# Kernel tuning notes

Hardware: AMD Instinct MI355X
Metric: run time of the kernel (lower is better)

## Reference

```python
import jax, jax.numpy as jnp
import numpy as np

T_LEN, E_LEN, BATCH, DIM = 32, 256, 16, 512  # topic_len, exp_len, batch, input=hidden size
HID = 512


def setup_inputs() -> dict:
    key = jax.random.key(0)
    k1, k2, k3, k4, k5, k6 = jax.random.split(key, 6)
    topic = jax.random.normal(k1, (T_LEN, BATCH, DIM), dtype=jnp.float32)
    exp_output = jax.random.normal(k2, (E_LEN, BATCH, DIM), dtype=jnp.float32)
    seq_mask = jax.random.bernoulli(k3, 0.1, (E_LEN, BATCH))  # True = masked exp position
    # nn.Linear(hidden+input, hidden): weight [HID, HID+DIM], bias [HID]
    lim1 = 1.0 / np.sqrt(HID + DIM)
    W_attn = jax.random.uniform(k4, (HID, HID + DIM), minval=-lim1, maxval=lim1, dtype=jnp.float32)
    b_attn = jax.random.uniform(k5, (HID,), minval=-lim1, maxval=lim1, dtype=jnp.float32)
    # nn.Linear(hidden, 1): weight [1, HID], bias [1]
    lim2 = 1.0 / np.sqrt(HID)
    kv, kb = jax.random.split(k6)
    v_score = jax.random.uniform(kv, (1, HID), minval=-lim2, maxval=lim2, dtype=jnp.float32)
    b_score = jax.random.uniform(kb, (1,), minval=-lim2, maxval=lim2, dtype=jnp.float32)
    return {"topic": topic, "exp_output": exp_output, "seq_mask": seq_mask,
            "W_attn": W_attn, "b_attn": b_attn, "v_score": v_score, "b_score": b_score}


def reference(topic, exp_output, seq_mask, W_attn, b_attn, v_score, b_score):
    # topic: [T, B, D]; exp_output: [E, B, D]; seq_mask: [E, B] bool
    D = topic.shape[2]
    # Split the concat-Linear: cat(topic, exp) @ W.T == topic @ W[:, :D].T + exp @ W[:, D:].T
    proj_t = jnp.einsum('tbd,hd->bth', topic, W_attn[:, :D])        # [B, T, H]
    proj_e = jnp.einsum('ebd,hd->beh', exp_output, W_attn[:, D:])   # [B, E, H]
    feat = jnp.tanh(proj_t[:, :, None, :] + proj_e[:, None, :, :] + b_attn)  # [B, T, E, H]
    energies = jnp.einsum('bteh,h->bte', feat, v_score[0]) + b_score[0]      # [B, T, E]
    # mask exp positions (broadcast over topic dim), as masked_fill(-1e12)
    energies = jnp.where(seq_mask.T[:, None, :], jnp.float32(-1e12), energies)
    attn_s1 = jax.nn.softmax(jnp.swapaxes(energies, 1, 2), axis=2)  # [B, E, T], softmax over topics
    attn_s2 = jax.nn.softmax(energies, axis=2)                      # [B, T, E], softmax over exp
    new_exp = jnp.einsum('bet,btd->bed', attn_s1, jnp.swapaxes(topic, 0, 1))       # [B, E, D]
    new_topic = jnp.einsum('bte,bed->btd', attn_s2, jnp.swapaxes(exp_output, 0, 1))  # [B, T, D]
    return new_topic, new_exp
```

## Files before the change

### kernel.cpp

```cpp
#include <hip/hip_runtime.h>
#include <hip/hip_bf16.h>
#include <cstddef>
#include <cstdint>

#define T_LEN 32
#define E_LEN 256
#define BATCH 16
#define DIM 512
#define HID 512
#define WROW 1024

#define TWO_LOG2E 2.8853900817779268f

typedef __attribute__((ext_vector_type(8))) short bf16x8;
typedef __attribute__((ext_vector_type(4))) float f32x4;

__device__ inline bf16x8 cvt8(float4 a, float4 b) {
    union { bf16x8 v; __hip_bfloat16 h[8]; } u;
    u.h[0] = __float2bfloat16(a.x); u.h[1] = __float2bfloat16(a.y);
    u.h[2] = __float2bfloat16(a.z); u.h[3] = __float2bfloat16(a.w);
    u.h[4] = __float2bfloat16(b.x); u.h[5] = __float2bfloat16(b.y);
    u.h[6] = __float2bfloat16(b.z); u.h[7] = __float2bfloat16(b.w);
    return u.v;
}

#define GPAD 8
#define GLDR (64 + GPAD)

__global__ __launch_bounds__(256) void gemm_fused(
    const float* __restrict__ topic, const float* __restrict__ expo,
    const float* __restrict__ W, const float* __restrict__ battn,
    float* __restrict__ EPT, float* __restrict__ EPE) {
    __shared__ __hip_bfloat16 As[64 * GLDR];
    __shared__ __hip_bfloat16 Bs[64 * GLDR];
    const int tid = threadIdx.x;
    const int by = blockIdx.y;
    const float* A; const float* Wp; const float* bias; float* C; int m0;
    if (by < 8) { A = topic; Wp = W;       bias = battn;   C = EPT; m0 = by * 64; }
    else        { A = expo;  Wp = W + DIM; bias = nullptr; C = EPE; m0 = (by - 8) * 64; }
    const int n0 = blockIdx.x * 64;
    const int w = tid >> 6;
    const int lane = tid & 63;
    const int l15 = lane & 15;
    const int g = lane >> 4;
    const int srow = tid >> 2;
    const int sc = tid & 3;

    f32x4 acc[4];
    const f32x4 z = {0.f, 0.f, 0.f, 0.f};
#pragma unroll
    for (int nt = 0; nt < 4; ++nt) acc[nt] = z;

    const float* ga = A + (size_t)(m0 + srow) * 512 + sc * 8;
    const float* gb = Wp + (size_t)(n0 + srow) * WROW + sc * 8;

    float4 a0 = *(const float4*)(ga);
    float4 a1 = *(const float4*)(ga + 4);
    float4 a2 = *(const float4*)(ga + 32);
    float4 a3 = *(const float4*)(ga + 36);
    float4 b0 = *(const float4*)(gb);
    float4 b1 = *(const float4*)(gb + 4);
    float4 b2 = *(const float4*)(gb + 32);
    float4 b3 = *(const float4*)(gb + 36);

    for (int kk = 0; kk < 8; ++kk) {
        bf16x8 av0 = cvt8(a0, a1), av1 = cvt8(a2, a3);
        bf16x8 bv0 = cvt8(b0, b1), bv1 = cvt8(b2, b3);
        if (kk < 7) {
            ga += 64; gb += 64;
            a0 = *(const float4*)(ga);
            a1 = *(const float4*)(ga + 4);
            a2 = *(const float4*)(ga + 32);
            a3 = *(const float4*)(ga + 36);
            b0 = *(const float4*)(gb);
            b1 = *(const float4*)(gb + 4);
            b2 = *(const float4*)(gb + 32);
            b3 = *(const float4*)(gb + 36);
        }
        __syncthreads();
        *(bf16x8*)&As[srow * GLDR + sc * 8] = av0;
        *(bf16x8*)&As[srow * GLDR + sc * 8 + 32] = av1;
        *(bf16x8*)&Bs[srow * GLDR + sc * 8] = bv0;
        *(bf16x8*)&Bs[srow * GLDR + sc * 8 + 32] = bv1;
        __syncthreads();
#pragma unroll
        for (int s = 0; s < 2; ++s) {
            bf16x8 af = *(const bf16x8*)&As[(w * 16 + l15) * GLDR + (s * 4 + g) * 8];
#pragma unroll
            for (int nt = 0; nt < 4; ++nt) {
                bf16x8 bf = *(const bf16x8*)&Bs[(nt * 16 + l15) * GLDR + (s * 4 + g) * 8];
                acc[nt] = __builtin_amdgcn_mfma_f32_16x16x32_bf16(af, bf, acc[nt], 0, 0, 0);
            }
        }
    }
#pragma unroll
    for (int nt = 0; nt < 4; ++nt) {
        int n = n0 + nt * 16 + l15;
        float bv = bias ? bias[n] : 0.f;
#pragma unroll
        for (int r = 0; r < 4; ++r) {
            int m = m0 + w * 16 + g * 4 + r;
            C[(size_t)m * 512 + n] = __builtin_amdgcn_exp2f((acc[nt][r] + bv) * TWO_LOG2E);
        }
    }
}

__global__ __launch_bounds__(256) void energies_k(const float* __restrict__ EPT,
                                                  const float* __restrict__ EPE,
                                                  const float* __restrict__ v,
                                                  const float* __restrict__ bscore,
                                                  const int* __restrict__ mask,
                                                  float* __restrict__ EN) {
    const int b = blockIdx.x;
    const int tg = blockIdx.y;
    const int ech = blockIdx.z;
    const int lane = threadIdx.x & 63;
    const int w = threadIdx.x >> 6;
    const int h0 = lane * 8;

    float sv[8], spt[4][8];
    float sumv;
    {
        float4 v0 = *(const float4*)(v + h0);
        float4 v1 = *(const float4*)(v + h0 + 4);
        float vr[8] = {v0.x, v0.y, v0.z, v0.w, v1.x, v1.y, v1.z, v1.w};
        float s = 0.f;
#pragma unroll
        for (int j = 0; j < 8; ++j) { sv[j] = -2.f * vr[j]; s += vr[j]; }
#pragma unroll
        for (int off = 32; off; off >>= 1) s += __shfl_xor(s, off);
        sumv = s;
#pragma unroll
        for (int i = 0; i < 4; ++i) {
            const float* p = EPT + ((size_t)((tg * 4 + i) * BATCH + b)) * HID + h0;
            float4 p0 = *(const float4*)(p);
            float4 p1 = *(const float4*)(p + 4);
            spt[i][0] = p0.x; spt[i][1] = p0.y; spt[i][2] = p0.z; spt[i][3] = p0.w;
            spt[i][4] = p1.x; spt[i][5] = p1.y; spt[i][6] = p1.z; spt[i][7] = p1.w;
        }
    }
    const int e0 = ech * 16 + w * 4;
    const float bs = bscore[0];
#pragma unroll
    for (int ei = 0; ei < 4; ++ei) {
        const int e = e0 + ei;
        const float* pe = EPE + ((size_t)(e * BATCH + b)) * HID + h0;
        float4 p0 = *(const float4*)(pe);
        float4 p1 = *(const float4*)(pe + 4);
        float pr[8] = {p0.x, p0.y, p0.z, p0.w, p1.x, p1.y, p1.z, p1.w};
        float acc[4] = {0.f, 0.f, 0.f, 0.f};
#pragma unroll
        for (int i = 0; i < 4; ++i) {
#pragma unroll
            for (int j = 0; j < 8; ++j) {
                float q = fmaf(spt[i][j], pr[j], 1.0f);
                float r = __builtin_amdgcn_rcpf(q);
                acc[i] = fmaf(sv[j], r, acc[i]);
            }
        }
#pragma unroll
        for (int i = 0; i < 4; ++i) {
#pragma unroll
            for (int off = 32; off; off >>= 1) acc[i] += __shfl_xor(acc[i], off);
        }
        if (lane == 0) {
            const int msk = mask[e * BATCH + b];
#pragma unroll
            for (int i = 0; i < 4; ++i) {
                float en = sumv + bs + acc[i];
                if (msk != 0) en = -1e12f;
                EN[((size_t)b * T_LEN + tg * 4 + i) * E_LEN + e] = en;
            }
        }
    }
}

__global__ __launch_bounds__(256) void epilogue_k(const float* __restrict__ EN,
                                                  const float* __restrict__ topic,
                                                  const float* __restrict__ expo,
                                                  float* __restrict__ out) {
    __shared__ float smem[4096];
    const int tid = threadIdx.x;
    const int lane = tid & 63;
    const int w = tid >> 6;
    if (blockIdx.x < 256) {
        const int b = blockIdx.x >> 4;
        const int e0 = (blockIdx.x & 15) * 16 + w * 4;
        float wv[4];
#pragma unroll
        for (int ei = 0; ei < 4; ++ei) {
            const int e = e0 + ei;
            float x = (lane < T_LEN) ? EN[((size_t)b * T_LEN + lane) * E_LEN + e] : -3e38f;
            float m = x;
#pragma unroll
            for (int off = 16; off; off >>= 1) m = fmaxf(m, __shfl_xor(m, off));
            float p = (lane < T_LEN) ? __expf(x - m) : 0.f;
            float s = p;
#pragma unroll
            for (int off = 16; off; off >>= 1) s += __shfl_xor(s, off);
            wv[ei] = __fdividef(p, s);
        }
        float acc[4][8] = {};
        const int d0 = lane * 8;
        for (int tc = 0; tc < 4; ++tc) {
            __syncthreads();
            {
                int f = tid * 16;
                int r = f >> 9;
                int d = f & 511;
                const float* src = topic + ((size_t)(tc * 8 + r) * BATCH + b) * DIM + d;
                float4 s0 = *(const float4*)(src);
                float4 s1 = *(const float4*)(src + 4);
                float4 s2 = *(const float4*)(src + 8);
                float4 s3 = *(const float4*)(src + 12);
                *(float4*)&smem[r * 512 + d] = s0;
                *(float4*)&smem[r * 512 + d + 4] = s1;
                *(float4*)&smem[r * 512 + d + 8] = s2;
                *(float4*)&smem[r * 512 + d + 12] = s3;
            }
            __syncthreads();
#pragma unroll
            for (int t8 = 0; t8 < 8; ++t8) {
                const int t = tc * 8 + t8;
                float4 r0 = *(const float4*)&smem[t8 * 512 + d0];
                float4 r1 = *(const float4*)&smem[t8 * 512 + d0 + 4];
                float wt[4];
#pragma unroll
                for (int ei = 0; ei < 4; ++ei) wt[ei] = __shfl(wv[ei], t);
#pragma unroll
                for (int ei = 0; ei < 4; ++ei) {
                    acc[ei][0] = fmaf(wt[ei], r0.x, acc[ei][0]);
                    acc[ei][1] = fmaf(wt[ei], r0.y, acc[ei][1]);
                    acc[ei][2] = fmaf(wt[ei], r0.z, acc[ei][2]);
                    acc[ei][3] = fmaf(wt[ei], r0.w, acc[ei][3]);
                    acc[ei][4] = fmaf(wt[ei], r1.x, acc[ei][4]);
                    acc[ei][5] = fmaf(wt[ei], r1.y, acc[ei][5]);
                    acc[ei][6] = fmaf(wt[ei], r1.z, acc[ei][6]);
                    acc[ei][7] = fmaf(wt[ei], r1.w, acc[ei][7]);
                }
            }
        }
#pragma unroll
        for (int ei = 0; ei < 4; ++ei) {
            float* o = out + (size_t)BATCH * T_LEN * DIM +
                       ((size_t)b * E_LEN + e0 + ei) * DIM + d0;
            *(float4*)(o) = *(float4*)&acc[ei][0];
            *(float4*)(o + 4) = *(float4*)&acc[ei][4];
        }
    } else {
        const int q = blockIdx.x - 256;
        const int b = q >> 5;
        const int tg = (q >> 1) & 15;
        const int bq = q >> 5;
        const int tg8 = (q >> 2) & 7;
        const int half = q & 1;
        const int bb = q >> 4;
        const int tgq = (q >> 1) & 7;
        const int hf = q & 1;
        (void)b; (void)tg; (void)bq; (void)tg8; (void)half;
        const int t = tgq * 4 + w;
        const int bt = bb * T_LEN + t;
        float4 xv = *(const float4*)&EN[(size_t)bt * E_LEN + lane * 4];
        float m = fmaxf(fmaxf(xv.x, xv.y), fmaxf(xv.z, xv.w));
#pragma unroll
        for (int off = 32; off; off >>= 1) m = fmaxf(m, __shfl_xor(m, off));
        float p0 = __expf(xv.x - m), p1 = __expf(xv.y - m);
        float p2 = __expf(xv.z - m), p3 = __expf(xv.w - m);
        float s = p0 + p1 + p2 + p3;
#pragma unroll
        for (int off = 32; off; off >>= 1) s += __shfl_xor(s, off);
        float inv = __fdividef(1.f, s);
        float4 wvv = {p0 * inv, p1 * inv, p2 * inv, p3 * inv};
        *(float4*)&smem[w * 256 + lane * 4] = wvv;
        __syncthreads();
        const int dglob = hf * 256 + tid;
        const float* base = expo + (size_t)bb * DIM + dglob;
        float a0 = 0.f, a1 = 0.f, a2 = 0.f, a3 = 0.f;
#pragma unroll 8
        for (int e = 0; e < E_LEN; ++e) {
            float rv = base[(size_t)e * BATCH * DIM];
            a0 = fmaf(smem[e], rv, a0);
            a1 = fmaf(smem[256 + e], rv, a1);
            a2 = fmaf(smem[512 + e], rv, a2);
            a3 = fmaf(smem[768 + e], rv, a3);
        }
        float* o = out + ((size_t)bb * T_LEN + tgq * 4) * DIM + dglob;
        o[0] = a0;
        o[DIM] = a1;
        o[2 * DIM] = a2;
        o[3 * DIM] = a3;
    }
}

extern "C" void kernel_launch(void* const* d_in, const int* in_sizes, int n_in,
                              void* d_out, int out_size, void* d_ws, size_t ws_size,
                              hipStream_t stream) {
    const float* topic = (const float*)d_in[0];
    const float* expo  = (const float*)d_in[1];
    const int*   mask  = (const int*)d_in[2];
    const float* W     = (const float*)d_in[3];
    const float* battn = (const float*)d_in[4];
    const float* vsc   = (const float*)d_in[5];
    const float* bsc   = (const float*)d_in[6];
    float* out = (float*)d_out;

    float* EPT = (float*)d_ws;
    float* EPE = EPT + (size_t)T_LEN * BATCH * HID;
    float* EN  = EPE + (size_t)E_LEN * BATCH * HID;

    gemm_fused<<<dim3(8, 72), 256, 0, stream>>>(topic, expo, W, battn, EPT, EPE);
    energies_k<<<dim3(BATCH, 8, 16), 256, 0, stream>>>(EPT, EPE, vsc, bsc, mask, EN);
    epilogue_k<<<512, 256, 0, stream>>>(EN, topic, expo, out);
}
```

Before: 120.3 us.

## Skip masked energies and rebalance epilogue work across more blocks

The energies kernel loads the mask up front and skips the tanh/reduction work for masked exp positions, writing -1e12 directly. The epilogue grid doubles to 1024 blocks. new_exp blocks split the D dimension in half and read topic straight from global memory instead of staging it in LDS. new_topic blocks handle 2 topics, split the E reduction across waves, and combine the partial sums through shared memory. This trades more blocks and extra global reads for better parallelism and less wasted compute on the roughly 10% of positions that are masked.

```diff
diff --git a/kernel.cpp b/kernel.cpp
--- a/kernel.cpp
+++ b/kernel.cpp
@@ -117,6 +117,11 @@
     const int lane = threadIdx.x & 63;
     const int w = threadIdx.x >> 6;
     const int h0 = lane * 8;
+    const int e0 = ech * 16 + w * 4;
+
+    int mk[4];
+#pragma unroll
+    for (int ei = 0; ei < 4; ++ei) mk[ei] = mask[(e0 + ei) * BATCH + b];
 
     float sv[8], spt[4][8];
     float sumv;
@@ -139,11 +144,18 @@
             spt[i][4] = p1.x; spt[i][5] = p1.y; spt[i][6] = p1.z; spt[i][7] = p1.w;
         }
     }
-    const int e0 = ech * 16 + w * 4;
     const float bs = bscore[0];
 #pragma unroll
     for (int ei = 0; ei < 4; ++ei) {
         const int e = e0 + ei;
+        if (mk[ei] != 0) {
+            if (lane == 0) {
+#pragma unroll
+                for (int i = 0; i < 4; ++i)
+                    EN[((size_t)b * T_LEN + tg * 4 + i) * E_LEN + e] = -1e12f;
+            }
+            continue;
+        }
         const float* pe = EPE + ((size_t)(e * BATCH + b)) * HID + h0;
         float4 p0 = *(const float4*)(pe);
         float4 p1 = *(const float4*)(pe + 4);
@@ -164,12 +176,9 @@
             for (int off = 32; off; off >>= 1) acc[i] += __shfl_xor(acc[i], off);
         }
         if (lane == 0) {
-            const int msk = mask[e * BATCH + b];
 #pragma unroll
             for (int i = 0; i < 4; ++i) {
-                float en = sumv + bs + acc[i];
-                if (msk != 0) en = -1e12f;
-                EN[((size_t)b * T_LEN + tg * 4 + i) * E_LEN + e] = en;
+                EN[((size_t)b * T_LEN + tg * 4 + i) * E_LEN + e] = sumv + bs + acc[i];
             }
         }
     }
@@ -179,13 +188,15 @@
                                                   const float* __restrict__ topic,
                                                   const float* __restrict__ expo,
                                                   float* __restrict__ out) {
-    __shared__ float smem[4096];
+    __shared__ float smem[2560];
     const int tid = threadIdx.x;
     const int lane = tid & 63;
     const int w = tid >> 6;
-    if (blockIdx.x < 256) {
-        const int b = blockIdx.x >> 4;
-        const int e0 = (blockIdx.x & 15) * 16 + w * 4;
+    if (blockIdx.x < 512) {
+        const int b = blockIdx.x >> 5;
+        const int ech = (blockIdx.x >> 1) & 15;
+        const int hf = blockIdx.x & 1;
+        const int e0 = ech * 16 + w * 4;
         float wv[4];
 #pragma unroll
         for (int ei = 0; ei < 4; ++ei) {
@@ -200,95 +211,76 @@
             for (int off = 16; off; off >>= 1) s += __shfl_xor(s, off);
             wv[ei] = __fdividef(p, s);
         }
-        float acc[4][8] = {};
-        const int d0 = lane * 8;
-        for (int tc = 0; tc < 4; ++tc) {
-            __syncthreads();
-            {
-                int f = tid * 16;
-                int r = f >> 9;
-                int d = f & 511;
-                const float* src = topic + ((size_t)(tc * 8 + r) * BATCH + b) * DIM + d;
-                float4 s0 = *(const float4*)(src);
-                float4 s1 = *(const float4*)(src + 4);
-                float4 s2 = *(const float4*)(src + 8);
-                float4 s3 = *(const float4*)(src + 12);
-                *(float4*)&smem[r * 512 + d] = s0;
-                *(float4*)&smem[r * 512 + d + 4] = s1;
-                *(float4*)&smem[r * 512 + d + 8] = s2;
-                *(float4*)&smem[r * 512 + d + 12] = s3;
-            }
-            __syncthreads();
-#pragma unroll
-            for (int t8 = 0; t8 < 8; ++t8) {
-                const int t = tc * 8 + t8;
-                float4 r0 = *(const float4*)&smem[t8 * 512 + d0];
-                float4 r1 = *(const float4*)&smem[t8 * 512 + d0 + 4];
-                float wt[4];
-#pragma unroll
-                for (int ei = 0; ei < 4; ++ei) wt[ei] = __shfl(wv[ei], t);
-#pragma unroll
-                for (int ei = 0; ei < 4; ++ei) {
-                    acc[ei][0] = fmaf(wt[ei], r0.x, acc[ei][0]);
-                    acc[ei][1] = fmaf(wt[ei], r0.y, acc[ei][1]);
-                    acc[ei][2] = fmaf(wt[ei], r0.z, acc[ei][2]);
-                    acc[ei][3] = fmaf(wt[ei], r0.w, acc[ei][3]);
-                    acc[ei][4] = fmaf(wt[ei], r1.x, acc[ei][4]);
-                    acc[ei][5] = fmaf(wt[ei], r1.y, acc[ei][5]);
-                    acc[ei][6] = fmaf(wt[ei], r1.z, acc[ei][6]);
-                    acc[ei][7] = fmaf(wt[ei], r1.w, acc[ei][7]);
-                }
+        const int d0 = hf * 256 + lane * 4;
+        float4 acc[4];
+#pragma unroll
+        for (int ei = 0; ei < 4; ++ei) acc[ei] = {0.f, 0.f, 0.f, 0.f};
+        for (int t = 0; t < T_LEN; ++t) {
+            float4 r = *(const float4*)(topic + ((size_t)t * BATCH + b) * DIM + d0);
+            float wt[4];
+#pragma unroll
+            for (int ei = 0; ei < 4; ++ei) wt[ei] = __shfl(wv[ei], t);
+#pragma unroll
+            for (int ei = 0; ei < 4; ++ei) {
+                acc[ei].x = fmaf(wt[ei], r.x, acc[ei].x);
+                acc[ei].y = fmaf(wt[ei], r.y, acc[ei].y);
+                acc[ei].z = fmaf(wt[ei], r.z, acc[ei].z);
+                acc[ei].w = fmaf(wt[ei], r.w, acc[ei].w);
             }
         }
 #pragma unroll
         for (int ei = 0; ei < 4; ++ei) {
             float* o = out + (size_t)BATCH * T_LEN * DIM +
                        ((size_t)b * E_LEN + e0 + ei) * DIM + d0;
-            *(float4*)(o) = *(float4*)&acc[ei][0];
-            *(float4*)(o + 4) = *(float4*)&acc[ei][4];
+            *(float4*)o = acc[ei];
         }
     } else {
-        const int q = blockIdx.x - 256;
+        const int q = blockIdx.x - 512;
         const int b = q >> 5;
-        const int tg = (q >> 1) & 15;
-        const int bq = q >> 5;
-        const int tg8 = (q >> 2) & 7;
-        const int half = q & 1;
-        const int bb = q >> 4;
-        const int tgq = (q >> 1) & 7;
+        const int tp = (q >> 1) & 15;
         const int hf = q & 1;
-        (void)b; (void)tg; (void)bq; (void)tg8; (void)half;
-        const int t = tgq * 4 + w;
-        const int bt = bb * T_LEN + t;
-        float4 xv = *(const float4*)&EN[(size_t)bt * E_LEN + lane * 4];
-        float m = fmaxf(fmaxf(xv.x, xv.y), fmaxf(xv.z, xv.w));
-#pragma unroll
-        for (int off = 32; off; off >>= 1) m = fmaxf(m, __shfl_xor(m, off));
-        float p0 = __expf(xv.x - m), p1 = __expf(xv.y - m);
-        float p2 = __expf(xv.z - m), p3 = __expf(xv.w - m);
-        float s = p0 + p1 + p2 + p3;
-#pragma unroll
-        for (int off = 32; off; off >>= 1) s += __shfl_xor(s, off);
-        float inv = __fdividef(1.f, s);
-        float4 wvv = {p0 * inv, p1 * inv, p2 * inv, p3 * inv};
-        *(float4*)&smem[w * 256 + lane * 4] = wvv;
+        if (w < 2) {
+            const int bt = b * T_LEN + tp * 2 + w;
+            float4 xv = *(const float4*)&EN[(size_t)bt * E_LEN + lane * 4];
+            float m = fmaxf(fmaxf(xv.x, xv.y), fmaxf(xv.z, xv.w));
+#pragma unroll
+            for (int off = 32; off; off >>= 1) m = fmaxf(m, __shfl_xor(m, off));
+            float p0 = __expf(xv.x - m), p1 = __expf(xv.y - m);
+            float p2 = __expf(xv.z - m), p3 = __expf(xv.w - m);
+            float s = p0 + p1 + p2 + p3;
+#pragma unroll
+            for (int off = 32; off; off >>= 1) s += __shfl_xor(s, off);
+            float inv = __fdividef(1.f, s);
+            float4 wvv = {p0 * inv, p1 * inv, p2 * inv, p3 * inv};
+            *(float4*)&smem[w * 256 + lane * 4] = wvv;
+        }
         __syncthreads();
-        const int dglob = hf * 256 + tid;
-        const float* base = expo + (size_t)bb * DIM + dglob;
-        float a0 = 0.f, a1 = 0.f, a2 = 0.f, a3 = 0.f;
-#pragma unroll 8
-        for (int e = 0; e < E_LEN; ++e) {
-            float rv = base[(size_t)e * BATCH * DIM];
-            a0 = fmaf(smem[e], rv, a0);
-            a1 = fmaf(smem[256 + e], rv, a1);
-            a2 = fmaf(smem[512 + e], rv, a2);
-            a3 = fmaf(smem[768 + e], rv, a3);
-        }
-        float* o = out + ((size_t)bb * T_LEN + tgq * 4) * DIM + dglob;
-        o[0] = a0;
-        o[DIM] = a1;
-        o[2 * DIM] = a2;
-        o[3 * DIM] = a3;
+        const int dl = lane * 4;
+        const int dglob = hf * 256 + dl;
+        float4 a0 = {0.f, 0.f, 0.f, 0.f};
+        float4 a1 = {0.f, 0.f, 0.f, 0.f};
+        const float* base = expo + (size_t)b * DIM + dglob;
+        for (int ee = 0; ee < 64; ++ee) {
+            const int e = w * 64 + ee;
+            float4 rv = *(const float4*)(base + (size_t)e * BATCH * DIM);
+            float w0 = smem[e];
+            float w1 = smem[256 + e];
+            a0.x = fmaf(w0, rv.x, a0.x); a0.y = fmaf(w0, rv.y, a0.y);
+            a0.z = fmaf(w0, rv.z, a0.z); a0.w = fmaf(w0, rv.w, a0.w);
+            a1.x = fmaf(w1, rv.x, a1.x); a1.y = fmaf(w1, rv.y, a1.y);
+            a1.z = fmaf(w1, rv.z, a1.z); a1.w = fmaf(w1, rv.w, a1.w);
+        }
+        *(float4*)&smem[512 + (w * 2 + 0) * 256 + dl] = a0;
+        *(float4*)&smem[512 + (w * 2 + 1) * 256 + dl] = a1;
+        __syncthreads();
+#pragma unroll
+        for (int tt = 0; tt < 2; ++tt) {
+            float sum = smem[512 + (0 * 2 + tt) * 256 + tid] +
+                        smem[512 + (1 * 2 + tt) * 256 + tid] +
+                        smem[512 + (2 * 2 + tt) * 256 + tid] +
+                        smem[512 + (3 * 2 + tt) * 256 + tid];
+            out[((size_t)b * T_LEN + tp * 2 + tt) * DIM + hf * 256 + tid] = sum;
+        }
     }
 }
 
@@ -310,5 +302,5 @@
 
     gemm_fused<<<dim3(8, 72), 256, 0, stream>>>(topic, expo, W, battn, EPT, EPE);
     energies_k<<<dim3(BATCH, 8, 16), 256, 0, stream>>>(EPT, EPE, vsc, bsc, mask, EN);
-    epilogue_k<<<512, 256, 0, stream>>>(EN, topic, expo, out);
-}
+    epilogue_k<<<1024, 256, 0, stream>>>(EN, topic, expo, out);
+}
```

Result: faster. 115.4 us (-4.1%).
